# Optimization experiments

Hardware: AMD Instinct MI355X
Metric: run time of the kernel (lower is better)

The kernel has to match this reference:

```python
import jax, jax.numpy as jnp
import numpy as np

B, N, H, NH, P = 32, 400, 512, 8, 3
DK = H // NH
SCALE = DK ** -0.5
EPS = 1e-5


def _ln(x, g, b):
    m = jnp.mean(x, axis=-1, keepdims=True)
    v = jnp.mean((x - m) ** 2, axis=-1, keepdims=True)
    return (x - m) * jax.lax.rsqrt(v + EPS) * g + b


def _split(x):  # [B,N,H] -> [B,h,N,dk]
    return x.reshape(x.shape[0], x.shape[1], NH, DK).transpose(0, 2, 1, 3)


def _merge(x):  # [B,h,N,dk] -> [B,N,H]
    return x.transpose(0, 2, 1, 3).reshape(x.shape[0], x.shape[2], H)


def _attn(q, k, v, mask):
    s = jnp.einsum('bhid,bhjd->bhij', q, k) * SCALE
    s = s * (1.0 + mask[:, None])  # learned multiplicative prior mask
    p = jax.nn.softmax(s, axis=-1)
    return jnp.einsum('bhij,bhjd->bhid', p, v)


def _weight_gen(pri, z, C, wq, keys, wf, bf):
    # pooled token query attends over the num_priors prior matrices
    qv = jnp.mean(z @ wq, axis=1)  # [B,H]
    aw = jax.nn.softmax((qv @ keys.T) * (H ** -0.5), axis=-1)  # [B,P]
    w = jnp.einsum('bp,bpij->bij', aw, pri)  # [B,N,N] fused prior mask
    fused = jnp.einsum('bij,bjh->bih', C, z) @ wf + bf  # [B,N,H] neighborhood fusion
    return w, aw, fused


def _ffn(x, w1, b1, w2, b2):
    return jax.nn.gelu(x @ w1 + b1, approximate=False) @ w2 + b2


def _forward(x_FC, x_SC, pri_FC, pri_SC, FC, SC, dw,
             ln_attn_FC_g, ln_attn_FC_b, ln_attn_SC_g, ln_attn_SC_b,
             ln_ffn_FC_g, ln_ffn_FC_b, ln_ffn_SC_g, ln_ffn_SC_b,
             qkv_FC_w, qkv_SC_w,
             ffn_FC_w1, ffn_FC_b1, ffn_FC_w2, ffn_FC_b2,
             ffn_SC_w1, ffn_SC_b1, ffn_SC_w2, ffn_SC_b2,
             wg_q_w, wg_keys, wg_fuse_w, wg_fuse_b,
             dist_in_FC_w, dist_in_FC_b, dist_in_SC_w, dist_in_SC_b,
             dist_out_FC_w, dist_out_FC_b, dist_out_SC_w, dist_out_SC_b):
    z_FC = _ln(x_FC, ln_attn_FC_g, ln_attn_FC_b)
    z_SC = _ln(x_SC, ln_attn_SC_g, ln_attn_SC_b)
    q_FC, k_FC, v_FC = [_split(t) for t in jnp.split(z_FC @ qkv_FC_w, 3, axis=-1)]
    q_SC, k_SC, v_SC = [_split(t) for t in jnp.split(z_SC @ qkv_SC_w, 3, axis=-1)]
    w_FC, aw_FC, fused_FC = _weight_gen(pri_FC, z_FC, FC, wg_q_w, wg_keys, wg_fuse_w, wg_fuse_b)
    w_SC, aw_SC, fused_SC = _weight_gen(pri_SC, z_SC, SC, wg_q_w, wg_keys, wg_fuse_w, wg_fuse_b)
    ctx_FC = _merge(_attn(q_FC, k_FC, v_FC, w_FC))
    ctx_SC = _merge(_attn(q_SC, k_SC, v_SC, w_SC))
    attn_out_FC = x_FC + ctx_FC + fused_FC
    attn_out_SC = x_SC + ctx_SC + fused_SC
    x_FC_new = attn_out_FC + _ffn(_ln(attn_out_FC, ln_ffn_FC_g, ln_ffn_FC_b), ffn_FC_w1, ffn_FC_b1, ffn_FC_w2, ffn_FC_b2)
    x_SC_new = attn_out_SC + _ffn(_ln(attn_out_SC, ln_ffn_SC_g, ln_ffn_SC_b), ffn_SC_w1, ffn_SC_b1, ffn_SC_w2, ffn_SC_b2)
    wf, ws = dw[0], dw[1]
    proj_FC = x_FC_new @ dist_in_FC_w + dist_in_FC_b
    proj_SC = x_SC_new @ dist_in_SC_w + dist_in_SC_b
    l_FC = jax.nn.log_softmax(proj_FC.reshape(-1, H), axis=-1)
    l_SC = jax.nn.log_softmax(proj_SC.reshape(-1, H), axis=-1)
    p_FC = jnp.exp(l_FC)
    p_SC = jnp.exp(l_SC)
    rows = jnp.float32(l_FC.shape[0])
    kl_FC = jnp.sum(p_SC * (l_SC - l_FC)) / rows  # KLDiv(batchmean)(l_FC, p_SC)
    kl_SC = jnp.sum(p_FC * (l_FC - l_SC)) / rows
    x_FC_out = (1.0 - wf) * x_FC_new + wf * (proj_FC @ dist_out_FC_w + dist_out_FC_b)
    x_SC_out = (1.0 - ws) * x_SC_new + ws * (proj_SC @ dist_out_SC_w + dist_out_SC_b)
    distill_loss = 0.5 * (kl_FC * wf + kl_SC * ws)
    return (x_FC_out, x_SC_out, distill_loss, aw_FC, aw_SC)


def setup_inputs() -> dict:
    key = jax.random.key(0)
    ks = jax.random.split(key, 24)
    init = lambda k, shape: 0.02 * jax.random.normal(k, shape, jnp.float32)
    d = {}
    d['x_FC'] = jax.random.normal(ks[0], (B, N, H), jnp.float32)
    d['x_SC'] = jax.random.normal(ks[1], (B, N, H), jnp.float32)
    d['pri_FC'] = jax.random.uniform(ks[2], (B, P, N, N), jnp.float32)
    d['pri_SC'] = jax.random.uniform(ks[3], (B, P, N, N), jnp.float32)
    d['FC'] = jax.random.uniform(ks[4], (B, N, N), jnp.float32)
    d['SC'] = jax.random.uniform(ks[5], (B, N, N), jnp.float32)
    d['dw'] = jnp.array([0.5, 0.5], jnp.float32)
    for nm in ['ln_attn_FC', 'ln_attn_SC', 'ln_ffn_FC', 'ln_ffn_SC']:
        d[nm + '_g'] = jnp.ones((H,), jnp.float32)
        d[nm + '_b'] = jnp.zeros((H,), jnp.float32)
    d['qkv_FC_w'] = init(ks[6], (H, 3 * H))
    d['qkv_SC_w'] = init(ks[7], (H, 3 * H))
    d['ffn_FC_w1'] = init(ks[8], (H, 4 * H)); d['ffn_FC_b1'] = jnp.zeros((4 * H,), jnp.float32)
    d['ffn_FC_w2'] = init(ks[9], (4 * H, H)); d['ffn_FC_b2'] = jnp.zeros((H,), jnp.float32)
    d['ffn_SC_w1'] = init(ks[10], (H, 4 * H)); d['ffn_SC_b1'] = jnp.zeros((4 * H,), jnp.float32)
    d['ffn_SC_w2'] = init(ks[11], (4 * H, H)); d['ffn_SC_b2'] = jnp.zeros((H,), jnp.float32)
    d['wg_q_w'] = init(ks[12], (H, H))
    d['wg_keys'] = init(ks[13], (P, H))
    d['wg_fuse_w'] = init(ks[14], (H, H)); d['wg_fuse_b'] = jnp.zeros((H,), jnp.float32)
    d['dist_in_FC_w'] = init(ks[15], (H, H)); d['dist_in_FC_b'] = jnp.zeros((H,), jnp.float32)
    d['dist_in_SC_w'] = init(ks[16], (H, H)); d['dist_in_SC_b'] = jnp.zeros((H,), jnp.float32)
    d['dist_out_FC_w'] = init(ks[17], (H, H)); d['dist_out_FC_b'] = jnp.zeros((H,), jnp.float32)
    d['dist_out_SC_w'] = init(ks[18], (H, H)); d['dist_out_SC_b'] = jnp.zeros((H,), jnp.float32)
    return d


def reference(x_FC, x_SC, pri_FC, pri_SC, FC, SC, dw,
              ln_attn_FC_g, ln_attn_FC_b, ln_attn_SC_g, ln_attn_SC_b,
              ln_ffn_FC_g, ln_ffn_FC_b, ln_ffn_SC_g, ln_ffn_SC_b,
              qkv_FC_w, qkv_SC_w,
              ffn_FC_w1, ffn_FC_b1, ffn_FC_w2, ffn_FC_b2,
              ffn_SC_w1, ffn_SC_b1, ffn_SC_w2, ffn_SC_b2,
              wg_q_w, wg_keys, wg_fuse_w, wg_fuse_b,
              dist_in_FC_w, dist_in_FC_b, dist_in_SC_w, dist_in_SC_b,
              dist_out_FC_w, dist_out_FC_b, dist_out_SC_w, dist_out_SC_b):
    return _forward(x_FC, x_SC, pri_FC, pri_SC, FC, SC, dw,
                    ln_attn_FC_g, ln_attn_FC_b, ln_attn_SC_g, ln_attn_SC_b,
                    ln_ffn_FC_g, ln_ffn_FC_b, ln_ffn_SC_g, ln_ffn_SC_b,
                    qkv_FC_w, qkv_SC_w,
                    ffn_FC_w1, ffn_FC_b1, ffn_FC_w2, ffn_FC_b2,
                    ffn_SC_w1, ffn_SC_b1, ffn_SC_w2, ffn_SC_b2,
                    wg_q_w, wg_keys, wg_fuse_w, wg_fuse_b,
                    dist_in_FC_w, dist_in_FC_b, dist_in_SC_w, dist_in_SC_b,
                    dist_out_FC_w, dist_out_FC_b, dist_out_SC_w, dist_out_SC_b)
```

## Files before the change

kernel.cpp:

```cpp
#include <hip/hip_runtime.h>
#include <hip/hip_bf16.h>
#include <math.h>

typedef __hip_bfloat16 bf16;

#define B_  32
#define N_  400
#define H_  512
#define NH_ 8
#define DK_ 64
#define P_  3
#define BN_ (B_*N_)
#define H3_ 1536
#define H4_ 2048

#define GLD16(g, l) __builtin_amdgcn_global_load_lds( \
    (__attribute__((address_space(1))) void*)(g), \
    (__attribute__((address_space(3))) void*)(l), 16, 0, 0)

__device__ __forceinline__ float b2f(bf16 v){ return __bfloat162float(v); }
__device__ __forceinline__ bf16  f2b(float v){ return __float2bfloat16(v); }
__device__ __forceinline__ float bfu(unsigned short u){ return __uint_as_float(((unsigned int)u)<<16); }
__device__ __forceinline__ unsigned short f2bu(float v){
  union { bf16 b; unsigned short u; } cv; cv.b = __float2bfloat16(v); return cv.u;
}
__device__ __forceinline__ bool is_f32(const void* gref){
  return *(const unsigned int*)gref == 0x3F800000u;
}
__device__ __forceinline__ float ldRaw(const void* p, long i, bool f32){
  return f32 ? ((const float*)p)[i] : b2f(((const bf16*)p)[i]);
}
__device__ __forceinline__ void stRaw(void* p, long i, float v, bool f32){
  if (f32) ((float*)p)[i] = v; else ((bf16*)p)[i] = f2b(v);
}

__device__ __forceinline__ float waveSum(float v){
  #pragma unroll
  for (int o=32;o>0;o>>=1) v += __shfl_xor(v,o,64);
  return v;
}
__device__ __forceinline__ float waveMax(float v){
  #pragma unroll
  for (int o=32;o>0;o>>=1) v = fmaxf(v,__shfl_xor(v,o,64));
  return v;
}
__device__ __forceinline__ float blockSum(float v, float* wred){
  v = waveSum(v);
  int w = threadIdx.x>>6, l = threadIdx.x&63;
  if (l==0) wred[w]=v;
  __syncthreads();
  float r = wred[0]+wred[1]+wred[2]+wred[3];
  __syncthreads();
  return r;
}
__device__ __forceinline__ float blockMax(float v, float* wred){
  v = waveMax(v);
  int w = threadIdx.x>>6, l = threadIdx.x&63;
  if (l==0) wred[w]=v;
  __syncthreads();
  float r = fmaxf(fmaxf(wred[0],wred[1]),fmaxf(wred[2],wred[3]));
  __syncthreads();
  return r;
}

template<int XMODE>
__global__ __launch_bounds__(256)
void ln_kernel(const void* __restrict__ x, const void* __restrict__ g,
               const void* __restrict__ bb, bf16* __restrict__ out,
               const void* __restrict__ gref)
{
  __shared__ float wred[4];
  const bool F32 = is_f32(gref);
  long row = blockIdx.x;
  int t = threadIdx.x;
  long base = row*H_;
  float v0, v1;
  if (XMODE==0){ v0 = ldRaw(x, base+t, F32); v1 = ldRaw(x, base+t+256, F32); }
  else         { v0 = b2f(((const bf16*)x)[base+t]); v1 = b2f(((const bf16*)x)[base+t+256]); }
  float mean = blockSum(v0+v1, wred) * (1.f/512.f);
  float d0 = v0-mean, d1 = v1-mean;
  float var = blockSum(d0*d0+d1*d1, wred) * (1.f/512.f);
  float rs = rsqrtf(var + 1e-5f);
  bf16* orow = out + base;
  orow[t]     = f2b(d0*rs*ldRaw(g,t,F32)     + ldRaw(bb,t,F32));
  orow[t+256] = f2b(d1*rs*ldRaw(g,t+256,F32) + ldRaw(bb,t+256,F32));
}

__global__ __launch_bounds__(256)
void tconv_kernel(const float* __restrict__ W, bf16* __restrict__ WT, int K, int N)
{
  __shared__ float tile[32][33];
  int n0 = blockIdx.x*32, k0 = blockIdx.y*32;
  int t = threadIdx.x;
  int c = t & 31, r = t >> 5;
  #pragma unroll
  for (int p=0;p<4;++p){
    int k = r + p*8;
    tile[k][c] = W[(long)(k0+k)*N + n0 + c];
  }
  __syncthreads();
  #pragma unroll
  for (int p=0;p<4;++p){
    int nn = r + p*8;
    WT[(long)(n0+nn)*K + k0 + c] = f2b(tile[c][nn]);
  }
}

__global__ __launch_bounds__(256)
void ztrans_kernel(const bf16* __restrict__ ZB, bf16* __restrict__ ZBT)
{
  __shared__ unsigned short tile[32][33];
  int j0 = blockIdx.x*32, h0 = blockIdx.y*32, b = blockIdx.z;
  int t = threadIdx.x;
  int c = t & 31, r = t >> 5;
  const unsigned short* src = (const unsigned short*)(ZB + (long)b*N_*H_);
  #pragma unroll
  for (int p=0;p<4;++p){
    int j = j0 + r + p*8;
    unsigned short v = 0;
    if (j < 400) v = src[(long)j*H_ + h0 + c];
    tile[r+p*8][c] = v;
  }
  __syncthreads();
  unsigned short* dst = (unsigned short*)(ZBT + (long)b*512*416);
  #pragma unroll
  for (int p=0;p<4;++p){
    int hh = r + p*8;
    dst[(long)(h0+hh)*416 + j0 + c] = tile[c][hh];
  }
}

__global__ __launch_bounds__(256)
void vtrans_kernel(const bf16* __restrict__ qkv, bf16* __restrict__ vtg)
{
  __shared__ unsigned short tile[32][33];
  int j0 = blockIdx.x*32, d0 = blockIdx.y*32, bh = blockIdx.z;
  int b = bh >> 3, h = bh & 7;
  int t = threadIdx.x;
  int c = t & 31, r = t >> 5;
  const unsigned short* src = (const unsigned short*)(qkv + (long)b*N_*H3_ + 1024 + h*64 + d0);
  #pragma unroll
  for (int p=0;p<4;++p){
    int j = j0 + r + p*8;
    unsigned short v = 0;
    if (j < 400) v = src[(long)j*H3_ + c];
    tile[r+p*8][c] = v;
  }
  __syncthreads();
  unsigned short* dst = (unsigned short*)(vtg + (long)bh*64*416);
  #pragma unroll
  for (int p=0;p<4;++p){
    int dd = r + p*8;
    dst[(long)(d0+dd)*416 + j0 + c] = tile[c][dd];
  }
}

template<int MI,int AMODE,int ACT,int RES,int OMODE>
__global__ __launch_bounds__(256)
void mgemm_kernel(const void* __restrict__ A, const bf16* __restrict__ BT,
                  const float* __restrict__ bias, const bf16* __restrict__ res,
                  void* __restrict__ out, long oOff,
                  int M, int Kl, int Kr, int Nn,
                  long sA, long sW, long sO,
                  const float* __restrict__ dwp, int dwidx)
{
  typedef __attribute__((ext_vector_type(8))) short bf16x8;
  typedef __attribute__((ext_vector_type(4))) float f32x4;
  constexpr int BM = MI*32;
  __shared__ unsigned short As[2][BM*32];
  __shared__ unsigned short Bs[2][128*32];
  int t = threadIdx.x;
  int w = t >> 6, l = t & 63;
  int wm = (w >> 1)*(MI*16), wn = (w & 1)*64;
  int m0 = blockIdx.y*BM, n0 = blockIdx.x*128;
  long zA = (long)blockIdx.z*sA;
  const bf16* Bb = BT + (long)blockIdx.z*sW;
  long zO = (long)blockIdx.z*sO;
  f32x4 acc[MI][4] = {};
  int lrow = l & 15, lkc = l >> 4;
  int srow = t >> 2, skc = t & 3;
  int nk = Kl >> 5;
  int buf = 0;

  if (AMODE==0){
    #pragma unroll
    for (int half=0; half<MI/2; ++half){
      const unsigned short* gA = (const unsigned short*)A + zA + (long)(m0+srow+half*64)*Kr + skc*8;
      GLD16(gA, &As[0][w*512 + half*2048]);
    }
    #pragma unroll
    for (int half=0; half<2; ++half){
      const unsigned short* gB = (const unsigned short*)Bb + (long)(n0+srow+half*64)*Kl + skc*8;
      GLD16(gB, &Bs[0][w*512 + half*2048]);
    }
    __syncthreads();
    for (int kt=0; kt<nk; ++kt){
      if (kt+1 < nk){
        int k1 = (kt+1) << 5;
        #pragma unroll
        for (int half=0; half<MI/2; ++half){
          const unsigned short* gA = (const unsigned short*)A + zA + (long)(m0+srow+half*64)*Kr + k1 + skc*8;
          GLD16(gA, &As[buf^1][w*512 + half*2048]);
        }
        #pragma unroll
        for (int half=0; half<2; ++half){
          const unsigned short* gB = (const unsigned short*)Bb + (long)(n0+srow+half*64)*Kl + k1 + skc*8;
          GLD16(gB, &Bs[buf^1][w*512 + half*2048]);
        }
      }
      bf16x8 af[MI], bf_[4];
      #pragma unroll
      for (int i=0;i<MI;++i) af[i]  = *(const bf16x8*)&As[buf][(wm + i*16 + lrow)*32 + lkc*8];
      #pragma unroll
      for (int i=0;i<4;++i)  bf_[i] = *(const bf16x8*)&Bs[buf][(wn + i*16 + lrow)*32 + lkc*8];
      #pragma unroll
      for (int mi=0;mi<MI;++mi)
        #pragma unroll
        for (int ni=0;ni<4;++ni)
          acc[mi][ni] = __builtin_amdgcn_mfma_f32_16x16x32_bf16(bf_[ni], af[mi], acc[mi][ni], 0, 0, 0);
      __syncthreads();
      buf ^= 1;
    }
  } else {
    for (int kt=0; kt<nk; ++kt){
      int k0 = kt << 5;
      #pragma unroll
      for (int half=0; half<MI/2; ++half){
        int row = srow + half*64;
        int gm = m0 + row;
        int gk = k0 + skc*8;
        uint4 va = make_uint4(0,0,0,0);
        if (gm < M && gk < Kr){
          const float* ap = (const float*)A + zA + (long)gm*Kr + gk;
          float4 f0 = *(const float4*)ap;
          float4 f1 = *(const float4*)(ap+4);
          union { uint4 u; unsigned short s[8]; } pv;
          pv.s[0]=f2bu(f0.x); pv.s[1]=f2bu(f0.y); pv.s[2]=f2bu(f0.z); pv.s[3]=f2bu(f0.w);
          pv.s[4]=f2bu(f1.x); pv.s[5]=f2bu(f1.y); pv.s[6]=f2bu(f1.z); pv.s[7]=f2bu(f1.w);
          va = pv.u;
        }
        *(uint4*)&As[0][row*32 + skc*8] = va;
      }
      #pragma unroll
      for (int half=0; half<2; ++half){
        int row = srow + half*64;
        uint4 vb = *(const uint4*)((const unsigned short*)Bb + (long)(n0+row)*Kl + k0 + skc*8);
        *(uint4*)&Bs[0][row*32 + skc*8] = vb;
      }
      __syncthreads();
      bf16x8 af[MI], bf_[4];
      #pragma unroll
      for (int i=0;i<MI;++i) af[i]  = *(const bf16x8*)&As[0][(wm + i*16 + lrow)*32 + lkc*8];
      #pragma unroll
      for (int i=0;i<4;++i)  bf_[i] = *(const bf16x8*)&Bs[0][(wn + i*16 + lrow)*32 + lkc*8];
      #pragma unroll
      for (int mi=0;mi<MI;++mi)
        #pragma unroll
        for (int ni=0;ni<4;++ni)
          acc[mi][ni] = __builtin_amdgcn_mfma_f32_16x16x32_bf16(bf_[ni], af[mi], acc[mi][ni], 0, 0, 0);
      __syncthreads();
    }
  }
  float wbl = (RES==2) ? dwp[dwidx] : 0.f;
  #pragma unroll
  for (int mi=0;mi<MI;++mi){
    int gm = m0 + wm + mi*16 + lrow;
    if (gm >= M) continue;
    #pragma unroll
    for (int ni=0;ni<4;++ni){
      int gnb = n0 + wn + ni*16 + lkc*4;
      long o = zO + (long)gm*Nn + gnb;
      float v0 = acc[mi][ni][0], v1 = acc[mi][ni][1], v2 = acc[mi][ni][2], v3 = acc[mi][ni][3];
      if (bias){
        float4 bv = *(const float4*)&bias[gnb];
        v0 += bv.x; v1 += bv.y; v2 += bv.z; v3 += bv.w;
      }
      if (ACT==1){
        v0 = 0.5f*v0*(1.f + erff(v0*0.70710678118654752f));
        v1 = 0.5f*v1*(1.f + erff(v1*0.70710678118654752f));
        v2 = 0.5f*v2*(1.f + erff(v2*0.70710678118654752f));
        v3 = 0.5f*v3*(1.f + erff(v3*0.70710678118654752f));
      }
      if (RES==1){
        ushort4 r4 = *(const ushort4*)((const unsigned short*)res + o);
        v0 += bfu(r4.x); v1 += bfu(r4.y); v2 += bfu(r4.z); v3 += bfu(r4.w);
      }
      if (RES==2){
        ushort4 r4 = *(const ushort4*)((const unsigned short*)res + o);
        v0 = (1.f-wbl)*bfu(r4.x) + wbl*v0;
        v1 = (1.f-wbl)*bfu(r4.y) + wbl*v1;
        v2 = (1.f-wbl)*bfu(r4.z) + wbl*v2;
        v3 = (1.f-wbl)*bfu(r4.w) + wbl*v3;
      }
      if (OMODE==0){
        ushort4 o4;
        o4.x = f2bu(v0); o4.y = f2bu(v1); o4.z = f2bu(v2); o4.w = f2bu(v3);
        *(ushort4*)((unsigned short*)out + o) = o4;
      } else {
        *(float4*)((float*)out + oOff + o) = make_float4(v0,v1,v2,v3);
      }
    }
  }
}

__global__ __launch_bounds__(256)
void zbar_kernel(const bf16* __restrict__ Z, float* __restrict__ zbar)
{
  __shared__ float red[256];
  int hc = blockIdx.x, b = blockIdx.y;
  int t = threadIdx.x;
  int col = hc*64 + (t & 63), ns = t >> 6;
  const bf16* p = Z + (long)b*N_*H_ + (long)ns*100*H_ + col;
  float s = 0.f;
  for (int n=0;n<100;++n) s += b2f(p[(long)n*H_]);
  red[t] = s;
  __syncthreads();
  if (t < 64){
    float tot = red[t]+red[t+64]+red[t+128]+red[t+192];
    zbar[b*512 + hc*64 + t] = tot * (1.f/400.f);
  }
}

__global__ __launch_bounds__(256)
void qv_kernel(const float* __restrict__ zbar, const void* __restrict__ wq,
               float* __restrict__ qv, const void* __restrict__ gref)
{
  __shared__ float red[256];
  const bool F32 = is_f32(gref);
  int ch = blockIdx.x, b = blockIdx.y;
  int t = threadIdx.x;
  int col = ch*32 + (t & 31), ks = t >> 5;
  const float* zb = zbar + b*512;
  float s = 0.f;
  int k0 = ks*64;
  for (int k=0;k<64;++k)
    s = fmaf(zb[k0+k], ldRaw(wq, (long)(k0+k)*512 + col, F32), s);
  red[t] = s;
  __syncthreads();
  if (t < 32){
    float q = 0.f;
    #pragma unroll
    for (int i=0;i<8;++i) q += red[t + i*32];
    qv[b*512 + ch*32 + t] = q;
  }
}

__global__ __launch_bounds__(256)
void aw_kernel(const float* __restrict__ qv, const void* __restrict__ keys,
               float* __restrict__ awf, void* __restrict__ outbase, long offAw,
               const void* __restrict__ gref)
{
  __shared__ float wred[4];
  const bool F32 = is_f32(gref);
  int b = blockIdx.x, t = threadIdx.x;
  const float* q = qv + b*512;
  float lg[3];
  #pragma unroll
  for (int p=0;p<3;++p){
    float part = q[t]*ldRaw(keys, p*512+t, F32) + q[t+256]*ldRaw(keys, p*512+t+256, F32);
    lg[p] = blockSum(part, wred) * 0.04419417382415922f;
  }
  float m = fmaxf(lg[0], fmaxf(lg[1], lg[2]));
  float e0 = expf(lg[0]-m), e1 = expf(lg[1]-m), e2 = expf(lg[2]-m);
  float inv = 1.f/(e0+e1+e2);
  if (t<3){
    float a = (t==0?e0:(t==1?e1:e2))*inv;
    awf[b*3+t] = a;
    stRaw(outbase, offAw + b*3 + t, a, F32);
  }
}

__global__ __launch_bounds__(256)
void wcomb_kernel(const void* __restrict__ pri, const float* __restrict__ awf,
                  bf16* __restrict__ WM, const void* __restrict__ gref)
{
  const bool F32 = is_f32(gref);
  long u = (long)blockIdx.x*256 + threadIdx.x;
  long e0 = u*4;
  int b = (int)(e0 / 160000);
  long r = e0 - (long)b*160000;
  float a0 = awf[b*3+0], a1 = awf[b*3+1], a2 = awf[b*3+2];
  float o0,o1,o2,o3;
  if (F32){
    const float* p0 = (const float*)pri + (long)b*3*160000 + r;
    float4 a = *(const float4*)(p0);
    float4 c = *(const float4*)(p0 + 160000);
    float4 d = *(const float4*)(p0 + 320000);
    o0 = a0*a.x + a1*c.x + a2*d.x;
    o1 = a0*a.y + a1*c.y + a2*d.y;
    o2 = a0*a.z + a1*c.z + a2*d.z;
    o3 = a0*a.w + a1*c.w + a2*d.w;
  } else {
    const bf16* p0 = (const bf16*)pri + (long)b*3*160000 + r;
    ushort4 a = *(const ushort4*)(p0);
    ushort4 c = *(const ushort4*)(p0 + 160000);
    ushort4 d = *(const ushort4*)(p0 + 320000);
    o0 = a0*bfu(a.x) + a1*bfu(c.x) + a2*bfu(d.x);
    o1 = a0*bfu(a.y) + a1*bfu(c.y) + a2*bfu(d.y);
    o2 = a0*bfu(a.z) + a1*bfu(c.z) + a2*bfu(d.z);
    o3 = a0*bfu(a.w) + a1*bfu(c.w) + a2*bfu(d.w);
  }
  ushort4 o;
  o.x = f2bu(o0); o.y = f2bu(o1); o.z = f2bu(o2); o.w = f2bu(o3);
  *(ushort4*)(WM + e0) = o;
}

__global__ __launch_bounds__(64)
void attn_kernel(const bf16* __restrict__ qkv, const bf16* __restrict__ wm,
                 const bf16* __restrict__ vtg, bf16* __restrict__ ctx)
{
  typedef __attribute__((ext_vector_type(8))) short bf16x8;
  typedef __attribute__((ext_vector_type(4))) float f32x4;
  __shared__ unsigned short Pbuf[2][16*40];
  int h = blockIdx.x, b = blockIdx.y, qt = blockIdx.z;
  int l = threadIdx.x;
  int lr = l & 15, lg = l >> 4;
  int i0 = qt*16;
  const bf16* qb = qkv + (long)b*N_*H3_ + h*64;
  const bf16* kb = qb + 512;
  const bf16* wrow = wm + (long)b*N_*N_;
  const bf16* vt = vtg + (long)(b*NH_ + h)*64*416;
  bf16x8 qf0 = *(const bf16x8*)(qb + (long)(i0+lr)*H3_ + lg*8);
  bf16x8 qf1 = *(const bf16x8*)(qb + (long)(i0+lr)*H3_ + 32 + lg*8);
  f32x4 s[25];
  float lmax = -1e30f;
  #pragma unroll
  for (int kt=0; kt<25; ++kt){
    bf16x8 kf0 = *(const bf16x8*)(kb + (long)(kt*16+lr)*H3_ + lg*8);
    bf16x8 kf1 = *(const bf16x8*)(kb + (long)(kt*16+lr)*H3_ + 32 + lg*8);
    f32x4 st = {0.f,0.f,0.f,0.f};
    st = __builtin_amdgcn_mfma_f32_16x16x32_bf16(kf0, qf0, st, 0,0,0);
    st = __builtin_amdgcn_mfma_f32_16x16x32_bf16(kf1, qf1, st, 0,0,0);
    uint2 w4 = *(const uint2*)(wrow + (long)(i0+lr)*400 + kt*16 + lg*4);
    float w0 = bfu((unsigned short)(w4.x & 0xffffu));
    float w1 = bfu((unsigned short)(w4.x >> 16));
    float w2 = bfu((unsigned short)(w4.y & 0xffffu));
    float w3 = bfu((unsigned short)(w4.y >> 16));
    st[0] = st[0]*0.125f*(1.f+w0);
    st[1] = st[1]*0.125f*(1.f+w1);
    st[2] = st[2]*0.125f*(1.f+w2);
    st[3] = st[3]*0.125f*(1.f+w3);
    lmax = fmaxf(lmax, fmaxf(fmaxf(st[0],st[1]), fmaxf(st[2],st[3])));
    s[kt] = st;
  }
  lmax = fmaxf(lmax, __shfl_xor(lmax, 16));
  lmax = fmaxf(lmax, __shfl_xor(lmax, 32));
  float lsum = 0.f;
  #pragma unroll
  for (int kt=0; kt<25; ++kt){
    #pragma unroll
    for (int q=0;q<4;++q){
      float e = expf(s[kt][q] - lmax);
      float rv = bfu(f2bu(e));
      s[kt][q] = rv;
      lsum += rv;
    }
  }
  lsum += __shfl_xor(lsum, 16);
  lsum += __shfl_xor(lsum, 32);
  float inv = 1.f/lsum;
  f32x4 o[4] = {};
  #pragma unroll
  for (int w=0; w<13; ++w){
    int t0 = 2*w, t1 = 2*w+1;
    uint2 pk0, pk1;
    pk0.x = (unsigned)f2bu(s[t0][0]) | ((unsigned)f2bu(s[t0][1])<<16);
    pk0.y = (unsigned)f2bu(s[t0][2]) | ((unsigned)f2bu(s[t0][3])<<16);
    if (t1 < 25){
      pk1.x = (unsigned)f2bu(s[t1][0]) | ((unsigned)f2bu(s[t1][1])<<16);
      pk1.y = (unsigned)f2bu(s[t1][2]) | ((unsigned)f2bu(s[t1][3])<<16);
    } else { pk1.x = 0u; pk1.y = 0u; }
    unsigned short* pb = Pbuf[w & 1];
    *(uint2*)&pb[lr*40 + lg*4]      = pk0;
    *(uint2*)&pb[lr*40 + 16 + lg*4] = pk1;
    bf16x8 pa = *(const bf16x8*)&pb[lr*40 + lg*8];
    #pragma unroll
    for (int dt=0; dt<4; ++dt){
      bf16x8 vf = *(const bf16x8*)(vt + (long)(dt*16+lr)*416 + w*32 + lg*8);
      o[dt] = __builtin_amdgcn_mfma_f32_16x16x32_bf16(pa, vf, o[dt], 0,0,0);
    }
  }
  #pragma unroll
  for (int q=0;q<4;++q){
    float iv = __shfl(inv, lg*4 + q);
    #pragma unroll
    for (int dt=0;dt<4;++dt)
      ctx[(long)(b*N_ + i0 + lg*4 + q)*H_ + h*64 + dt*16 + lr] = f2b(o[dt][q]*iv);
  }
}

__global__ __launch_bounds__(256)
void addres_kernel(const void* __restrict__ x, const bf16* ctx,
                   const bf16* __restrict__ fu, bf16* aout,
                   const void* __restrict__ gref)
{
  const bool F32 = is_f32(gref);
  long u = ((long)blockIdx.x*256 + threadIdx.x)*4;
  float x0,x1,x2,x3;
  if (F32){
    float4 xv = *(const float4*)((const float*)x + u);
    x0=xv.x; x1=xv.y; x2=xv.z; x3=xv.w;
  } else {
    ushort4 xa = *(const ushort4*)((const bf16*)x + u);
    x0=bfu(xa.x); x1=bfu(xa.y); x2=bfu(xa.z); x3=bfu(xa.w);
  }
  ushort4 ca = *(const ushort4*)(ctx+u);
  ushort4 fa = *(const ushort4*)(fu+u);
  ushort4 o;
  o.x = f2bu(x0+bfu(ca.x)+bfu(fa.x));
  o.y = f2bu(x1+bfu(ca.y)+bfu(fa.y));
  o.z = f2bu(x2+bfu(ca.z)+bfu(fa.z));
  o.w = f2bu(x3+bfu(ca.w)+bfu(fa.w));
  *(ushort4*)(aout+u) = o;
}

__global__ __launch_bounds__(256)
void kl_rows_kernel(const bf16* __restrict__ pF, const bf16* __restrict__ pS,
                    float2* __restrict__ rowpart)
{
  __shared__ float wred[4];
  long row = blockIdx.x;
  int t = threadIdx.x;
  const bf16* fr = pF + row*512;
  const bf16* sr = pS + row*512;
  float f0 = b2f(fr[t]), f1 = b2f(fr[t+256]), s0 = b2f(sr[t]), s1 = b2f(sr[t+256]);
  float mF = blockMax(fmaxf(f0,f1), wred);
  float mS = blockMax(fmaxf(s0,s1), wred);
  float sumF = blockSum(expf(f0-mF)+expf(f1-mF), wred);
  float sumS = blockSum(expf(s0-mS)+expf(s1-mS), wred);
  float lseF = mF + logf(sumF), lseS = mS + logf(sumS);
  float lF0 = f0-lseF, lF1 = f1-lseF, lS0 = s0-lseS, lS1 = s1-lseS;
  float pS0 = expf(lS0), pS1 = expf(lS1), pF0 = expf(lF0), pF1 = expf(lF1);
  float a  = pS0*(lS0-lF0) + pS1*(lS1-lF1);
  float bb = pF0*(lF0-lS0) + pF1*(lF1-lS1);
  a  = blockSum(a,  wred);
  bb = blockSum(bb, wred);
  if (t==0) rowpart[row] = make_float2(a, bb);
}

__global__ __launch_bounds__(256)
void kl_final_kernel(const float2* __restrict__ rowpart, const void* __restrict__ dw,
                     void* __restrict__ outbase, long offLoss,
                     const void* __restrict__ gref)
{
  __shared__ float wred[4];
  const bool F32 = is_f32(gref);
  int t = threadIdx.x;
  float sa=0.f, sb=0.f;
  for (int i=t;i<BN_;i+=256){ float2 v = rowpart[i]; sa+=v.x; sb+=v.y; }
  sa = blockSum(sa, wred);
  sb = blockSum(sb, wred);
  if (t==0){
    float wf = ldRaw(dw,0,F32), ws = ldRaw(dw,1,F32);
    float loss = 0.5f*((sa/12800.f)*wf + (sb/12800.f)*ws);
    stRaw(outbase, offLoss, loss, F32);
  }
}

#define OFF_ZB    0L
#define OFF_QKV   13107200L
#define OFF_FUSED 52428800L
#define OFF_WM    65536000L
#define OFF_CZ    75776000L
#define OFF_PROJ0 88883200L
#define OFF_PROJ1 101990400L
#define OFF_QKVT  115097600L
#define OFF_W1T   116670464L
#define OFF_W2T   118767616L
#define OFF_FUT   120864768L
#define OFF_DIT   121389056L
#define OFF_DOT   121913344L
#define OFF_ZBT   122437632L
#define OFF_ZBAR  136069120L
#define OFF_AWF   136134656L
#define OFF_ROWP  136135680L
#define OFF_VTG   136238080L
#define OFF_QV    149869568L

extern "C" void kernel_launch(void* const* d_in, const int* in_sizes, int n_in,
                              void* d_out, int out_size, void* d_ws, size_t ws_size,
                              hipStream_t stream)
{
  (void)in_sizes; (void)n_in; (void)out_size; (void)ws_size;
  const void* x[2]    = {d_in[0],  d_in[1]};
  const void* pri[2]  = {d_in[2],  d_in[3]};
  const float* Cm[2]  = {(const float*)d_in[4], (const float*)d_in[5]};
  const float* dwf    =  (const float*)d_in[6];
  const void* lnag[2] = {d_in[7],  d_in[9]};
  const void* lnab[2] = {d_in[8],  d_in[10]};
  const void* lnfg[2] = {d_in[11], d_in[13]};
  const void* lnfb[2] = {d_in[12], d_in[14]};
  const float* qkvw[2]= {(const float*)d_in[15], (const float*)d_in[16]};
  const float* fw1[2] = {(const float*)d_in[17], (const float*)d_in[21]};
  const float* fb1[2] = {(const float*)d_in[18], (const float*)d_in[22]};
  const float* fw2[2] = {(const float*)d_in[19], (const float*)d_in[23]};
  const float* fb2[2] = {(const float*)d_in[20], (const float*)d_in[24]};
  const void* wgq     =  d_in[25];
  const void* wgk     =  d_in[26];
  const float* wgfw   =  (const float*)d_in[27];
  const float* wgfb   =  (const float*)d_in[28];
  const float* diw[2] = {(const float*)d_in[29], (const float*)d_in[31]};
  const float* dib[2] = {(const float*)d_in[30], (const float*)d_in[32]};
  const float* dow[2] = {(const float*)d_in[33], (const float*)d_in[35]};
  const float* dob[2] = {(const float*)d_in[34], (const float*)d_in[36]};
  const void* gref    =  d_in[7];

  char* ws = (char*)d_ws;
  bf16*  ZB    = (bf16*)(ws + OFF_ZB);
  bf16*  LN2   = (bf16*)(ws + OFF_ZB);
  bf16*  XNEW  = (bf16*)(ws + OFF_ZB);
  bf16*  QKV   = (bf16*)(ws + OFF_QKV);
  bf16*  HH    = (bf16*)(ws + OFF_QKV);
  bf16*  FUSED = (bf16*)(ws + OFF_FUSED);
  bf16*  WM    = (bf16*)(ws + OFF_WM);
  bf16*  CZ    = (bf16*)(ws + OFF_CZ);
  bf16*  CTX   = (bf16*)(ws + OFF_CZ);
  bf16*  AOUT  = (bf16*)(ws + OFF_CZ);
  bf16*  PROJ[2] = {(bf16*)(ws + OFF_PROJ0), (bf16*)(ws + OFF_PROJ1)};
  bf16*  QKVT  = (bf16*)(ws + OFF_QKVT);
  bf16*  W1T   = (bf16*)(ws + OFF_W1T);
  bf16*  W2T   = (bf16*)(ws + OFF_W2T);
  bf16*  FUT   = (bf16*)(ws + OFF_FUT);
  bf16*  DIT   = (bf16*)(ws + OFF_DIT);
  bf16*  DOT   = (bf16*)(ws + OFF_DOT);
  bf16*  ZBT   = (bf16*)(ws + OFF_ZBT);
  bf16*  VTG   = (bf16*)(ws + OFF_VTG);
  float* ZBAR  = (float*)(ws + OFF_ZBAR);
  float* AWF   = (float*)(ws + OFF_AWF);
  float2* ROWP = (float2*)(ws + OFF_ROWP);
  float* QV    = (float*)(ws + OFF_QV);

  const long offX[2]  = {0L, 6553600L};
  const long offLoss  = 13107200L;
  const long offAw[2] = {13107201L, 13107297L};

  for (int s=0; s<2; ++s){
    tconv_kernel<<<dim3(48,16),256,0,stream>>>(qkvw[s], QKVT, 512, 1536);
    tconv_kernel<<<dim3(64,16),256,0,stream>>>(fw1[s],  W1T,  512, 2048);
    tconv_kernel<<<dim3(16,64),256,0,stream>>>(fw2[s],  W2T,  2048, 512);
    tconv_kernel<<<dim3(16,16),256,0,stream>>>(wgfw,    FUT,  512, 512);
    tconv_kernel<<<dim3(16,16),256,0,stream>>>(diw[s],  DIT,  512, 512);
    tconv_kernel<<<dim3(16,16),256,0,stream>>>(dow[s],  DOT,  512, 512);
    ln_kernel<0><<<BN_,256,0,stream>>>(x[s], lnag[s], lnab[s], ZB, gref);
    zbar_kernel<<<dim3(8,B_),256,0,stream>>>(ZB, ZBAR);
    ztrans_kernel<<<dim3(13,16,32),256,0,stream>>>(ZB, ZBT);
    mgemm_kernel<4,0,0,0,0><<<dim3(12,100,1),256,0,stream>>>(
        ZB, QKVT, nullptr, nullptr, QKV, 0, BN_, 512, 512, H3_, 0,0,0, nullptr,0);
    vtrans_kernel<<<dim3(13,2,256),256,0,stream>>>(QKV, VTG);
    qv_kernel<<<dim3(16,B_),256,0,stream>>>(ZBAR, wgq, QV, gref);
    aw_kernel<<<B_,256,0,stream>>>(QV, wgk, AWF, d_out, offAw[s], gref);
    wcomb_kernel<<<5000,256,0,stream>>>(pri[s], AWF, WM, gref);
    mgemm_kernel<4,1,0,0,0><<<dim3(4,4,32),256,0,stream>>>(
        Cm[s], ZBT, nullptr, nullptr, CZ, 0, 400, 416, 400, 512,
        160000L, 212992L, 204800L, nullptr,0);
    mgemm_kernel<2,0,0,0,0><<<dim3(4,200,1),256,0,stream>>>(
        CZ, FUT, wgfb, nullptr, FUSED, 0, BN_, 512, 512, 512, 0,0,0, nullptr,0);
    attn_kernel<<<dim3(NH_,B_,25),64,0,stream>>>(QKV, WM, VTG, CTX);
    addres_kernel<<<6400,256,0,stream>>>(x[s], CTX, FUSED, AOUT, gref);
    ln_kernel<1><<<BN_,256,0,stream>>>(AOUT, lnfg[s], lnfb[s], LN2, gref);
    mgemm_kernel<4,0,1,0,0><<<dim3(16,100,1),256,0,stream>>>(
        LN2, W1T, fb1[s], nullptr, HH, 0, BN_, 512, 512, H4_, 0,0,0, nullptr,0);
    mgemm_kernel<2,0,0,1,0><<<dim3(4,200,1),256,0,stream>>>(
        HH, W2T, fb2[s], AOUT, XNEW, 0, BN_, 2048, 2048, 512, 0,0,0, nullptr,0);
    mgemm_kernel<2,0,0,0,0><<<dim3(4,200,1),256,0,stream>>>(
        XNEW, DIT, dib[s], nullptr, PROJ[s], 0, BN_, 512, 512, 512, 0,0,0, nullptr,0);
    mgemm_kernel<2,0,0,2,1><<<dim3(4,200,1),256,0,stream>>>(
        PROJ[s], DOT, dob[s], XNEW, d_out, offX[s], BN_, 512, 512, 512, 0,0,0, dwf, s);
  }
  kl_rows_kernel<<<BN_,256,0,stream>>>(PROJ[0], PROJ[1], ROWP);
  kl_final_kernel<<<1,256,0,stream>>>(ROWP, dwf, d_out, offLoss, gref);
}
```

Before: 1.011 ms.

## Fuse residual add into attention epilogue and switch to online softmax

```diff
diff --git a/kernel.cpp b/kernel.cpp
--- a/kernel.cpp
+++ b/kernel.cpp
@@ -407,11 +407,14 @@
 
 __global__ __launch_bounds__(64)
 void attn_kernel(const bf16* __restrict__ qkv, const bf16* __restrict__ wm,
-                 const bf16* __restrict__ vtg, bf16* __restrict__ ctx)
+                 const bf16* __restrict__ vtg, const void* __restrict__ x,
+                 const bf16* __restrict__ fused, bf16* __restrict__ aout,
+                 const void* __restrict__ gref)
 {
   typedef __attribute__((ext_vector_type(8))) short bf16x8;
   typedef __attribute__((ext_vector_type(4))) float f32x4;
   __shared__ unsigned short Pbuf[2][16*40];
+  const bool F32 = is_f32(gref);
   int h = blockIdx.x, b = blockIdx.y, qt = blockIdx.z;
   int l = threadIdx.x;
   int lr = l & 15, lg = l >> 4;
@@ -422,96 +425,92 @@
   const bf16* vt = vtg + (long)(b*NH_ + h)*64*416;
   bf16x8 qf0 = *(const bf16x8*)(qb + (long)(i0+lr)*H3_ + lg*8);
   bf16x8 qf1 = *(const bf16x8*)(qb + (long)(i0+lr)*H3_ + 32 + lg*8);
-  f32x4 s[25];
-  float lmax = -1e30f;
-  #pragma unroll
-  for (int kt=0; kt<25; ++kt){
-    bf16x8 kf0 = *(const bf16x8*)(kb + (long)(kt*16+lr)*H3_ + lg*8);
-    bf16x8 kf1 = *(const bf16x8*)(kb + (long)(kt*16+lr)*H3_ + 32 + lg*8);
-    f32x4 st = {0.f,0.f,0.f,0.f};
-    st = __builtin_amdgcn_mfma_f32_16x16x32_bf16(kf0, qf0, st, 0,0,0);
-    st = __builtin_amdgcn_mfma_f32_16x16x32_bf16(kf1, qf1, st, 0,0,0);
-    uint2 w4 = *(const uint2*)(wrow + (long)(i0+lr)*400 + kt*16 + lg*4);
-    float w0 = bfu((unsigned short)(w4.x & 0xffffu));
-    float w1 = bfu((unsigned short)(w4.x >> 16));
-    float w2 = bfu((unsigned short)(w4.y & 0xffffu));
-    float w3 = bfu((unsigned short)(w4.y >> 16));
-    st[0] = st[0]*0.125f*(1.f+w0);
-    st[1] = st[1]*0.125f*(1.f+w1);
-    st[2] = st[2]*0.125f*(1.f+w2);
-    st[3] = st[3]*0.125f*(1.f+w3);
-    lmax = fmaxf(lmax, fmaxf(fmaxf(st[0],st[1]), fmaxf(st[2],st[3])));
-    s[kt] = st;
-  }
-  lmax = fmaxf(lmax, __shfl_xor(lmax, 16));
-  lmax = fmaxf(lmax, __shfl_xor(lmax, 32));
-  float lsum = 0.f;
-  #pragma unroll
-  for (int kt=0; kt<25; ++kt){
-    #pragma unroll
-    for (int q=0;q<4;++q){
-      float e = expf(s[kt][q] - lmax);
-      float rv = bfu(f2bu(e));
-      s[kt][q] = rv;
-      lsum += rv;
-    }
-  }
-  lsum += __shfl_xor(lsum, 16);
-  lsum += __shfl_xor(lsum, 32);
-  float inv = 1.f/lsum;
+  float rm = -1e30f, rl = 0.f;
   f32x4 o[4] = {};
   #pragma unroll
   for (int w=0; w<13; ++w){
     int t0 = 2*w, t1 = 2*w+1;
-    uint2 pk0, pk1;
-    pk0.x = (unsigned)f2bu(s[t0][0]) | ((unsigned)f2bu(s[t0][1])<<16);
-    pk0.y = (unsigned)f2bu(s[t0][2]) | ((unsigned)f2bu(s[t0][3])<<16);
+    f32x4 s0, s1;
+    {
+      bf16x8 kf0 = *(const bf16x8*)(kb + (long)(t0*16+lr)*H3_ + lg*8);
+      bf16x8 kf1 = *(const bf16x8*)(kb + (long)(t0*16+lr)*H3_ + 32 + lg*8);
+      f32x4 st = {0.f,0.f,0.f,0.f};
+      st = __builtin_amdgcn_mfma_f32_16x16x32_bf16(kf0, qf0, st, 0,0,0);
+      st = __builtin_amdgcn_mfma_f32_16x16x32_bf16(kf1, qf1, st, 0,0,0);
+      uint2 w4 = *(const uint2*)(wrow + (long)(i0+lr)*400 + t0*16 + lg*4);
+      s0[0] = st[0]*0.125f*(1.f + bfu((unsigned short)(w4.x & 0xffffu)));
+      s0[1] = st[1]*0.125f*(1.f + bfu((unsigned short)(w4.x >> 16)));
+      s0[2] = st[2]*0.125f*(1.f + bfu((unsigned short)(w4.y & 0xffffu)));
+      s0[3] = st[3]*0.125f*(1.f + bfu((unsigned short)(w4.y >> 16)));
+    }
     if (t1 < 25){
-      pk1.x = (unsigned)f2bu(s[t1][0]) | ((unsigned)f2bu(s[t1][1])<<16);
-      pk1.y = (unsigned)f2bu(s[t1][2]) | ((unsigned)f2bu(s[t1][3])<<16);
-    } else { pk1.x = 0u; pk1.y = 0u; }
+      bf16x8 kf0 = *(const bf16x8*)(kb + (long)(t1*16+lr)*H3_ + lg*8);
+      bf16x8 kf1 = *(const bf16x8*)(kb + (long)(t1*16+lr)*H3_ + 32 + lg*8);
+      f32x4 st = {0.f,0.f,0.f,0.f};
+      st = __builtin_amdgcn_mfma_f32_16x16x32_bf16(kf0, qf0, st, 0,0,0);
+      st = __builtin_amdgcn_mfma_f32_16x16x32_bf16(kf1, qf1, st, 0,0,0);
+      uint2 w4 = *(const uint2*)(wrow + (long)(i0+lr)*400 + t1*16 + lg*4);
+      s1[0] = st[0]*0.125f*(1.f + bfu((unsigned short)(w4.x & 0xffffu)));
+      s1[1] = st[1]*0.125f*(1.f + bfu((unsigned short)(w4.x >> 16)));
+      s1[2] = st[2]*0.125f*(1.f + bfu((unsigned short)(w4.y & 0xffffu)));
+      s1[3] = st[3]*0.125f*(1.f + bfu((unsigned short)(w4.y >> 16)));
+    } else {
+      s1[0]=s1[1]=s1[2]=s1[3] = -1e30f;
+    }
+    float tm = fmaxf(fmaxf(fmaxf(s0[0],s0[1]), fmaxf(s0[2],s0[3])),
+                     fmaxf(fmaxf(s1[0],s1[1]), fmaxf(s1[2],s1[3])));
+    tm = fmaxf(tm, __shfl_xor(tm, 16));
+    tm = fmaxf(tm, __shfl_xor(tm, 32));
+    float mn = fmaxf(rm, tm);
+    float sc = expf(rm - mn);
+    unsigned pk0x, pk0y, pk1x = 0u, pk1y = 0u;
+    float ls = 0.f;
+    {
+      unsigned u0 = f2bu(expf(s0[0]-mn)), u1 = f2bu(expf(s0[1]-mn));
+      unsigned u2 = f2bu(expf(s0[2]-mn)), u3 = f2bu(expf(s0[3]-mn));
+      pk0x = u0 | (u1<<16); pk0y = u2 | (u3<<16);
+      ls += __uint_as_float(u0<<16) + __uint_as_float(u1<<16)
+          + __uint_as_float(u2<<16) + __uint_as_float(u3<<16);
+    }
+    if (t1 < 25){
+      unsigned u0 = f2bu(expf(s1[0]-mn)), u1 = f2bu(expf(s1[1]-mn));
+      unsigned u2 = f2bu(expf(s1[2]-mn)), u3 = f2bu(expf(s1[3]-mn));
+      pk1x = u0 | (u1<<16); pk1y = u2 | (u3<<16);
+      ls += __uint_as_float(u0<<16) + __uint_as_float(u1<<16)
+          + __uint_as_float(u2<<16) + __uint_as_float(u3<<16);
+    }
+    ls += __shfl_xor(ls, 16);
+    ls += __shfl_xor(ls, 32);
+    rl = rl*sc + ls;
+    rm = mn;
     unsigned short* pb = Pbuf[w & 1];
-    *(uint2*)&pb[lr*40 + lg*4]      = pk0;
-    *(uint2*)&pb[lr*40 + 16 + lg*4] = pk1;
+    *(uint2*)&pb[lr*40 + lg*4]      = make_uint2(pk0x, pk0y);
+    *(uint2*)&pb[lr*40 + 16 + lg*4] = make_uint2(pk1x, pk1y);
     bf16x8 pa = *(const bf16x8*)&pb[lr*40 + lg*8];
+    float sq0 = __shfl(sc, lg*4 + 0);
+    float sq1 = __shfl(sc, lg*4 + 1);
+    float sq2 = __shfl(sc, lg*4 + 2);
+    float sq3 = __shfl(sc, lg*4 + 3);
     #pragma unroll
     for (int dt=0; dt<4; ++dt){
+      o[dt][0] *= sq0; o[dt][1] *= sq1; o[dt][2] *= sq2; o[dt][3] *= sq3;
       bf16x8 vf = *(const bf16x8*)(vt + (long)(dt*16+lr)*416 + w*32 + lg*8);
       o[dt] = __builtin_amdgcn_mfma_f32_16x16x32_bf16(pa, vf, o[dt], 0,0,0);
     }
   }
+  float invl = 1.f/rl;
   #pragma unroll
   for (int q=0;q<4;++q){
-    float iv = __shfl(inv, lg*4 + q);
+    float iv = __shfl(invl, lg*4 + q);
+    long gi = (long)(b*N_ + i0 + lg*4 + q);
     #pragma unroll
-    for (int dt=0;dt<4;++dt)
-      ctx[(long)(b*N_ + i0 + lg*4 + q)*H_ + h*64 + dt*16 + lr] = f2b(o[dt][q]*iv);
-  }
-}
-
-__global__ __launch_bounds__(256)
-void addres_kernel(const void* __restrict__ x, const bf16* ctx,
-                   const bf16* __restrict__ fu, bf16* aout,
-                   const void* __restrict__ gref)
-{
-  const bool F32 = is_f32(gref);
-  long u = ((long)blockIdx.x*256 + threadIdx.x)*4;
-  float x0,x1,x2,x3;
-  if (F32){
-    float4 xv = *(const float4*)((const float*)x + u);
-    x0=xv.x; x1=xv.y; x2=xv.z; x3=xv.w;
-  } else {
-    ushort4 xa = *(const ushort4*)((const bf16*)x + u);
-    x0=bfu(xa.x); x1=bfu(xa.y); x2=bfu(xa.z); x3=bfu(xa.w);
-  }
-  ushort4 ca = *(const ushort4*)(ctx+u);
-  ushort4 fa = *(const ushort4*)(fu+u);
-  ushort4 o;
-  o.x = f2bu(x0+bfu(ca.x)+bfu(fa.x));
-  o.y = f2bu(x1+bfu(ca.y)+bfu(fa.y));
-  o.z = f2bu(x2+bfu(ca.z)+bfu(fa.z));
-  o.w = f2bu(x3+bfu(ca.w)+bfu(fa.w));
-  *(ushort4*)(aout+u) = o;
+    for (int dt=0;dt<4;++dt){
+      long oi = gi*H_ + h*64 + dt*16 + lr;
+      float xv = F32 ? ((const float*)x)[oi] : b2f(((const bf16*)x)[oi]);
+      float fv = b2f(fused[oi]);
+      aout[oi] = f2b(o[dt][q]*iv + xv + fv);
+    }
+  }
 }
 
 __global__ __launch_bounds__(256)
@@ -614,7 +613,6 @@
   bf16*  FUSED = (bf16*)(ws + OFF_FUSED);
   bf16*  WM    = (bf16*)(ws + OFF_WM);
   bf16*  CZ    = (bf16*)(ws + OFF_CZ);
-  bf16*  CTX   = (bf16*)(ws + OFF_CZ);
   bf16*  AOUT  = (bf16*)(ws + OFF_CZ);
   bf16*  PROJ[2] = {(bf16*)(ws + OFF_PROJ0), (bf16*)(ws + OFF_PROJ1)};
   bf16*  QKVT  = (bf16*)(ws + OFF_QKVT);
@@ -655,8 +653,7 @@
         160000L, 212992L, 204800L, nullptr,0);
     mgemm_kernel<2,0,0,0,0><<<dim3(4,200,1),256,0,stream>>>(
         CZ, FUT, wgfb, nullptr, FUSED, 0, BN_, 512, 512, 512, 0,0,0, nullptr,0);
-    attn_kernel<<<dim3(NH_,B_,25),64,0,stream>>>(QKV, WM, VTG, CTX);
-    addres_kernel<<<6400,256,0,stream>>>(x[s], CTX, FUSED, AOUT, gref);
+    attn_kernel<<<dim3(NH_,B_,25),64,0,stream>>>(QKV, WM, VTG, x[s], FUSED, AOUT, gref);
     ln_kernel<1><<<BN_,256,0,stream>>>(AOUT, lnfg[s], lnfb[s], LN2, gref);
     mgemm_kernel<4,0,1,0,0><<<dim3(16,100,1),256,0,stream>>>(
         LN2, W1T, fb1[s], nullptr, HH, 0, BN_, 512, 512, H4_, 0,0,0, nullptr,0);
```

New measurement: 1.001 ms. Within noise of the previous version (-0.9%).
